# Optimization experiments

Measured on AMD Instinct MI355X. Metric: run time of the kernel, lower is better.

The kernel has to match this reference:

```python
import jax, jax.numpy as jnp
import numpy as np
import math

SPARSITY = 0.5
EPS = 1e-5


def _quant(x, bit, after_relu):
    # mirrors torch quantize_per_tensor math; straight-through (torch mutates x.data)
    def q(x):
        mx, mn = x.max(), x.min()
        scale = (mx - mn) / (2 ** bit - 1)
        if after_relu:
            ir = jnp.clip(jnp.round(x / scale), 0.0, 2 ** bit - 1)
            return ir * scale
        zp_min = jnp.floor(mn / scale)
        return (jnp.round((x - mn) / scale) + zp_min) * scale
    return x + jax.lax.stop_gradient(q(x) - x)


def _subnet(scores, k):
    # GetSubnet: top-k mask of |scores| with straight-through gradient
    s = jnp.abs(scores)
    flat = s.ravel()
    j = int((1.0 - k) * flat.size)
    order = jnp.argsort(flat)
    mask = jnp.zeros_like(flat).at[order[j:]].set(1.0).reshape(s.shape)
    return jax.lax.stop_gradient(mask - s) + s


def _scale(hw_one, fan_in):
    std = math.sqrt(2.0) / math.sqrt(fan_in * 0.5)
    return hw_one.mean() / std


def _blend_w(scores, sign, hw_one, hw_zero):
    m = _subnet(scores, SPARSITY)
    return sign * (hw_one[0] * m + hw_zero[0] * (1.0 - m))


def _conv(x, w):
    return jax.lax.conv_general_dilated(x, w, (1, 1), 'VALID',
                                        dimension_numbers=('NCHW', 'OIHW', 'NCHW'))


def _maxpool2(x):
    return jax.lax.reduce_window(x, -jnp.inf, jax.lax.max,
                                 (1, 1, 2, 2), (1, 1, 2, 2), 'VALID')


def _bn(x):
    m = x.mean((0, 2, 3), keepdims=True)
    v = x.var((0, 2, 3), keepdims=True)
    return (x - m) / jnp.sqrt(v + EPS)


def setup_inputs() -> dict:
    key = jax.random.key(0)
    ks = jax.random.split(key, 16)
    B = 4096
    shapes = {
        '1': (64, 1, 3, 3),
        '2': (16, 64, 3, 3),
        '3': (128, 400),
        '4': (10, 128),
    }
    inp = {'x': jax.random.normal(ks[0], (B, 1, 28, 28), dtype=jnp.float32)}
    i = 1
    for name, shp in shapes.items():
        inp['scores' + name] = jax.random.normal(ks[i], shp, dtype=jnp.float32); i += 1
        inp['sign' + name] = jnp.sign(jax.random.normal(ks[i], shp, dtype=jnp.float32)); i += 1
        inp['hw' + name + '_one'] = jax.random.uniform(ks[i], (1,) + shp, dtype=jnp.float32); i += 1
        # hw_zero: small "off" conductances
        inp['hw' + name + '_zero'] = 0.05 * jax.random.uniform(jax.random.fold_in(ks[i], 1), (1,) + shp, dtype=jnp.float32)
    inp['qb'] = 8
    return inp


def reference(x, scores1, sign1, hw1_one, hw1_zero,
              scores2, sign2, hw2_one, hw2_zero,
              scores3, sign3, hw3_one, hw3_zero,
              scores4, sign4, hw4_one, hw4_zero, qb):
    x = _maxpool2(x)
    x = _quant(x, qb, False)
    # conv1 (fan_in = 1*3*3 = 9)
    w1 = _blend_w(scores1, sign1, hw1_one, hw1_zero)
    x = _conv(x, w1) / _scale(hw1_one, 9)
    x = jax.nn.relu(_bn(x))
    x = _quant(x, qb, True)
    # conv2 (fan_in = 64*9 = 576)
    w2 = _blend_w(scores2, sign2, hw2_one, hw2_zero)
    x = _conv(x, w2) / _scale(hw2_one, 576)
    x = _maxpool2(x)
    x = jax.nn.relu(_bn(x))
    x = _quant(x, qb, True)
    x = x.reshape(x.shape[0], -1)  # [B, 400]
    # fc1 (fan_in = 400)
    w3 = _blend_w(scores3, sign3, hw3_one, hw3_zero)
    x = (x @ w3.T) / _scale(hw3_one, 400)
    x = jax.nn.relu(x)
    x = _quant(x, qb, True)
    # fc2 (fan_in = 128)
    w4 = _blend_w(scores4, sign4, hw4_one, hw4_zero)
    x = (x @ w4.T) / _scale(hw4_one, 128)
    return jax.nn.log_softmax(x, axis=1)
```

## Files before the change

### kernel.cpp

```cpp
#include <hip/hip_runtime.h>
#include <hip/hip_bf16.h>
#include <math.h>

#define DEV __device__ __forceinline__

constexpr int BATCH = 4096;
constexpr int NBA = 512;
constexpr int NBB = 4096;
constexpr int NBC = 4096;
constexpr int NBE = 512;
constexpr int NBW = 16;

constexpr size_t OFF_POOLED = 0;
constexpr size_t OFF_Y2P = OFF_POOLED + (size_t)BATCH*196;
constexpr size_t OFF_ST1 = OFF_Y2P;
constexpr size_t OFF_H3  = OFF_Y2P + (size_t)BATCH*400;
constexpr size_t OFF_ST2 = OFF_H3;
constexpr size_t OFF_W2  = OFF_H3 + (size_t)BATCH*128;
constexpr size_t OFF_W3  = OFF_W2 + 9216;
constexpr size_t OFF_W4  = OFF_W3 + 51200;
constexpr size_t OFF_WSC = OFF_W4 + 1280;
constexpr size_t OFF_BN1 = OFF_WSC + 4;
constexpr size_t OFF_BN2 = OFF_BN1 + 256;
constexpr size_t OFF_GMM = OFF_BN2 + 64;
constexpr size_t OFF_ONS = OFF_GMM + 8;
constexpr size_t OFF_T   = OFF_ONS + 16;
constexpr size_t OFF_MMA = OFF_T + 4;
constexpr size_t OFF_HIST= OFF_MMA + 1024;
constexpr size_t OFF_W1M = OFF_HIST + 32768;
constexpr size_t OFF_SEL = OFF_W1M + 2048;
constexpr size_t OFF_H2G = OFF_SEL + 8;
constexpr size_t OFF_H3G = OFF_H2G + 4096;

typedef __attribute__((ext_vector_type(8))) short bf16x8;
typedef __attribute__((ext_vector_type(4))) float f32x4;

struct InPtrs {
  const float* x;
  const float* sc[4];
  const float* sg[4];
  const float* on[4];
  const float* ze[4];
  const int* qb;
};

__constant__ const int KW_L[16]  ={0,1,1,2,2,2,2,2,2,2,2,2,2,2,2,3};
__constant__ const int KW_S[16]  ={0,0,1,0,1,2,3,4,5,6,7,8,9,10,11,0};
__constant__ const int KW_NB[4]  ={1,2,12,1};
__constant__ const int KW_N[4]   ={576,9216,51200,1280};
__constant__ const int KW_FAN[4] ={9,576,400,128};
__constant__ const int KW_BW0[4] ={0,1,3,15};
__constant__ const int KW_BW1[4] ={1,3,15,16};

DEV unsigned fenc(float f){ unsigned u=__float_as_uint(f); return (u&0x80000000u)? ~u : (u|0x80000000u); }
DEV float fdec(unsigned e){ return __uint_as_float((e&0x80000000u)? (e&0x7fffffffu) : ~e); }
DEV unsigned short f2bf(float f){ unsigned u=__float_as_uint(f); return (unsigned short)((u + 0x7fffu + ((u>>16)&1u))>>16); }

DEV float blk_sum(float v, float* red, int t){
  red[t]=v; __syncthreads();
  for (int s=128;s>0;s>>=1){ if(t<s) red[t]+=red[t+s]; __syncthreads(); }
  float r=red[0]; __syncthreads();
  return r;
}
DEV float blk_min(float v, float* red, int t){
  red[t]=v; __syncthreads();
  for (int s=128;s>0;s>>=1){ if(t<s) red[t]=fminf(red[t],red[t+s]); __syncthreads(); }
  float r=red[0]; __syncthreads();
  return r;
}
DEV float blk_max(float v, float* red, int t){
  red[t]=v; __syncthreads();
  for (int s=128;s>0;s>>=1){ if(t<s) red[t]=fmaxf(red[t],red[t+s]); __syncthreads(); }
  float r=red[0]; __syncthreads();
  return r;
}

DEV int2 find256(const int* hist, int nbins, int kk, int t, int* suf, int* sh2){
  const int G=nbins>>8;
  const int lo=t*G;
  int g=0;
  for (int b=0;b<G;++b) g+=hist[lo+b];
  suf[t]=g; __syncthreads();
  for (int s=1;s<256;s<<=1){
    int add=(t+s<256)?suf[t+s]:0;
    __syncthreads();
    suf[t]+=add;
    __syncthreads();
  }
  const int S=suf[t];
  const int Snext=(t<255)?suf[t+1]:0;
  if (S>=kk && Snext<kk){
    int c2=Snext;
    for (int b=lo+G-1;b>=lo;--b){
      c2+=hist[b];
      if (c2>=kk){ sh2[0]=b; sh2[1]=kk-(c2-hist[b]); break; }
    }
  }
  __syncthreads();
  int2 r=make_int2(sh2[0],sh2[1]);
  __syncthreads();
  return r;
}

DEV void build_pat(unsigned* PAT, const unsigned short* qxs, int t){
  for (int pos=t; pos<144; pos+=256){
    int py=(pos*171)>>11;
    int px=pos-py*12;
    const unsigned short* q0=qxs+py*16+px;
    unsigned e0=q0[0],  e1=q0[1],  e2=q0[2];
    unsigned e3=q0[16], e4=q0[17], e5=q0[18];
    unsigned e6=q0[32], e7=q0[33], e8=q0[34];
    uint4* dst=(uint4*)(PAT+pos*20);
    dst[0]=make_uint4(e0|(e1<<16), e2|(e3<<16), e4|(e5<<16), e6|(e7<<16));
    dst[1]=make_uint4(e8, 0u, 0u, 0u);
    dst[2]=make_uint4(0u,0u,0u,0u);
    dst[3]=make_uint4(0u,0u,0u,0u);
  }
}

__global__ __launch_bounds__(256) void ka_kernel(InPtrs in, float* __restrict__ ws){
  const int t=threadIdx.x, blk=blockIdx.x;
  __shared__ int h[2048];
  __shared__ float red[256];
  if (blk<NBA){
    if (blk==0){
      unsigned* Z=(unsigned*)(ws+OFF_H2G);
      for (int i=t;i<8192;i+=256) Z[i]=0u;
    }
    const float* x=in.x;
    float* pooled=ws+OFF_POOLED;
    float lmn=3.4e38f, lmx=-3.4e38f;
    for (int p=blk*256+t; p<BATCH*196; p+=NBA*256){
      int b=p/196, r=p-b*196;
      int oy=r/14, ox=r-oy*14;
      const float* px=x+b*784+oy*56+ox*2;
      float m=fmaxf(fmaxf(px[0],px[1]),fmaxf(px[28],px[29]));
      pooled[p]=m;
      lmn=fminf(lmn,m); lmx=fmaxf(lmx,m);
    }
    float bmn=blk_min(lmn,red,t);
    float bmx=blk_max(lmx,red,t);
    if (t==0){ ws[OFF_MMA+blk*2]=bmn; ws[OFF_MMA+blk*2+1]=bmx; }
  } else {
    const int bw=blk-NBA;
    const int L=KW_L[bw], s=KW_S[bw], nb=KW_NB[L];
    const int n4=KW_N[L]>>2;
    const int lo=(int)(((long long)n4*s)/nb), hi=(int)(((long long)n4*(s+1))/nb);
    const float4* sc4=(const float4*)in.sc[L];
    const float4* on4=(const float4*)in.on[L];
    for (int i=t;i<2048;i+=256) h[i]=0;
    __syncthreads();
    float onsum=0.f;
    for (int i=lo+t;i<hi;i+=256){
      float4 v=sc4[i];
      atomicAdd(&h[(__float_as_uint(v.x)&0x7fffffffu)>>20],1);
      atomicAdd(&h[(__float_as_uint(v.y)&0x7fffffffu)>>20],1);
      atomicAdd(&h[(__float_as_uint(v.z)&0x7fffffffu)>>20],1);
      atomicAdd(&h[(__float_as_uint(v.w)&0x7fffffffu)>>20],1);
      float4 o=on4[i];
      onsum+=(o.x+o.y)+(o.z+o.w);
    }
    __syncthreads();
    unsigned* GH=(unsigned*)(ws+OFF_HIST);
    for (int i=t;i<2048;i+=256) GH[bw*2048+i]=(unsigned)h[i];
    float S=blk_sum(onsum,red,t);
    if (t==0) ws[OFF_ONS+bw]=S;
  }
}

__global__ __launch_bounds__(256) void kw2a_kernel(float* __restrict__ ws){
  const int t=threadIdx.x, L=blockIdx.x;
  __shared__ int hist[2048];
  __shared__ int suf[256];
  __shared__ int sh2[2];
  __shared__ float redm[256], redx[256];
  if (L==0){
    float a0=ws[OFF_MMA+2*t],       a1=ws[OFF_MMA+2*(t+256)];
    float b0=ws[OFF_MMA+2*t+1],     b1=ws[OFF_MMA+2*(t+256)+1];
    redm[t]=fminf(a0,a1); redx[t]=fmaxf(b0,b1);
    __syncthreads();
    for (int s=128;s>0;s>>=1){
      if (t<s){ redm[t]=fminf(redm[t],redm[t+s]); redx[t]=fmaxf(redx[t],redx[t+s]); }
      __syncthreads();
    }
    unsigned* U=(unsigned*)(ws+OFF_GMM);
    if (t==0){ U[0]=fenc(redm[0]); U[1]=fenc(redx[0]); }
    if (t>=2 && t<8) U[t]=(t&1)? 0u : 0xFFFFFFFFu;
    unsigned* z=(unsigned*)(ws+OFF_W1M);
    for (int i=t;i<2048;i+=256) z[i]=0u;
    __syncthreads();
  }
  const unsigned* GH=(const unsigned*)(ws+OFF_HIST);
  for (int i=t;i<2048;i+=256){
    int s=0;
    for (int bw=KW_BW0[L]; bw<KW_BW1[L]; ++bw) s+=(int)GH[bw*2048+i];
    hist[i]=s;
  }
  __syncthreads();
  int2 f1=find256(hist,2048,KW_N[L]>>1,t,suf,sh2);
  if (t==0){
    unsigned* SEL=(unsigned*)(ws+OFF_SEL);
    SEL[L*2]=(unsigned)f1.x; SEL[L*2+1]=(unsigned)f1.y;
  }
}

__global__ __launch_bounds__(256) void kwp2_kernel(InPtrs in, float* __restrict__ ws){
  const int t=threadIdx.x, bw=blockIdx.x;
  const int L=KW_L[bw], s=KW_S[bw], nb=KW_NB[L];
  const int n4=KW_N[L]>>2;
  const int lo=(int)(((long long)n4*s)/nb), hi=(int)(((long long)n4*(s+1))/nb);
  const unsigned b0=((const unsigned*)(ws+OFF_SEL))[L*2];
  const float4* sc4=(const float4*)in.sc[L];
  unsigned* GH2=(unsigned*)(ws+OFF_H2G)+L*1024;
  for (int i=lo+t;i<hi;i+=256){
    float4 v=sc4[i];
    unsigned ux=__float_as_uint(v.x)&0x7fffffffu;
    unsigned uy=__float_as_uint(v.y)&0x7fffffffu;
    unsigned uz=__float_as_uint(v.z)&0x7fffffffu;
    unsigned uw=__float_as_uint(v.w)&0x7fffffffu;
    if ((ux>>20)==b0) atomicAdd(&GH2[(ux>>10)&1023u],1u);
    if ((uy>>20)==b0) atomicAdd(&GH2[(uy>>10)&1023u],1u);
    if ((uz>>20)==b0) atomicAdd(&GH2[(uz>>10)&1023u],1u);
    if ((uw>>20)==b0) atomicAdd(&GH2[(uw>>10)&1023u],1u);
  }
}

__global__ __launch_bounds__(256) void kwp3_kernel(InPtrs in, float* __restrict__ ws){
  const int t=threadIdx.x, bw=blockIdx.x;
  const int L=KW_L[bw], s=KW_S[bw], nb=KW_NB[L];
  const int n4=KW_N[L]>>2;
  const int lo=(int)(((long long)n4*s)/nb), hi=(int)(((long long)n4*(s+1))/nb);
  const unsigned* SEL=(const unsigned*)(ws+OFF_SEL);
  const unsigned b0=SEL[L*2]; const int r1=(int)SEL[L*2+1];
  __shared__ int hist[1024];
  __shared__ int suf[256];
  __shared__ int sh2[2];
  const unsigned* GH2=(const unsigned*)(ws+OFF_H2G)+L*1024;
  for (int i=t;i<1024;i+=256) hist[i]=(int)GH2[i];
  __syncthreads();
  int2 f2=find256(hist,1024,r1,t,suf,sh2);
  const unsigned pre=(b0<<10)|(unsigned)f2.x;
  const float4* sc4=(const float4*)in.sc[L];
  unsigned* GH3=(unsigned*)(ws+OFF_H3G)+L*1024;
  for (int i=lo+t;i<hi;i+=256){
    float4 v=sc4[i];
    unsigned ux=__float_as_uint(v.x)&0x7fffffffu;
    unsigned uy=__float_as_uint(v.y)&0x7fffffffu;
    unsigned uz=__float_as_uint(v.z)&0x7fffffffu;
    unsigned uw=__float_as_uint(v.w)&0x7fffffffu;
    if ((ux>>10)==pre) atomicAdd(&GH3[ux&1023u],1u);
    if ((uy>>10)==pre) atomicAdd(&GH3[uy&1023u],1u);
    if ((uz>>10)==pre) atomicAdd(&GH3[uz&1023u],1u);
    if ((uw>>10)==pre) atomicAdd(&GH3[uw&1023u],1u);
  }
}

__global__ __launch_bounds__(256) void kw3_kernel(InPtrs in, float* __restrict__ ws){
  const int t=threadIdx.x, bw=blockIdx.x;
  const int L=KW_L[bw], s=KW_S[bw], nb=KW_NB[L];
  const int n4=KW_N[L]>>2;
  const int lo=(int)(((long long)n4*s)/nb), hi=(int)(((long long)n4*(s+1))/nb);
  const unsigned* SEL=(const unsigned*)(ws+OFF_SEL);
  const unsigned b0=SEL[L*2]; const int r1=(int)SEL[L*2+1];
  __shared__ int hist[1024];
  __shared__ int suf[256];
  __shared__ int sh2[2];
  const unsigned* GH2=(const unsigned*)(ws+OFF_H2G)+L*1024;
  for (int i=t;i<1024;i+=256) hist[i]=(int)GH2[i];
  __syncthreads();
  int2 f2=find256(hist,1024,r1,t,suf,sh2);
  const unsigned pre=(b0<<10)|(unsigned)f2.x;
  const int r2=f2.y;
  __syncthreads();
  const unsigned* GH3=(const unsigned*)(ws+OFF_H3G)+L*1024;
  for (int i=t;i<1024;i+=256) hist[i]=(int)GH3[i];
  __syncthreads();
  int2 f3=find256(hist,1024,r2,t,suf,sh2);
  const unsigned T=(pre<<10)|(unsigned)f3.x;
  if (s==0 && t==0){
    float os=0.f;
    for (int b=KW_BW0[L]; b<KW_BW1[L]; ++b) os+=ws[OFF_ONS+b];
    ws[OFF_WSC+L]=(os/(float)KW_N[L])*sqrtf((float)KW_FAN[L])*0.5f;
  }
  const float4* sc4=(const float4*)in.sc[L];
  const float4* sg4=(const float4*)in.sg[L];
  const float4* on4=(const float4*)in.on[L];
  const float4* ze4=(const float4*)in.ze[L];
  float* wout=ws+OFF_W4;
  unsigned* W3Fu=(unsigned*)(ws+OFF_W3);
  unsigned short* W1F=(unsigned short*)(ws+OFF_W1M);
  unsigned short* W2F=(unsigned short*)(ws+OFF_W2);
  for (int i4=lo+t;i4<hi;i4+=256){
    float4 sv4=sc4[i4], g=sg4[i4], o=on4[i4], z=ze4[i4];
    float sv[4]={sv4.x,sv4.y,sv4.z,sv4.w}, gv[4]={g.x,g.y,g.z,g.w};
    float ov[4]={o.x,o.y,o.z,o.w}, zv[4]={z.x,z.y,z.z,z.w};
    #pragma unroll
    for (int j=0;j<4;++j){
      int i=i4*4+j;
      unsigned u=__float_as_uint(sv[j])&0x7fffffffu;
      float w=gv[j]*((u>=T)? ov[j] : zv[j]);
      if (L==0){
        int oc=i/9; int k=i-oc*9;
        int ocT=oc>>4, ocL=oc&15, quad=k>>3, kj=k&7;
        unsigned short hb=f2bf(w);
        float lo2=w-__uint_as_float((unsigned)hb<<16);
        W1F[((((ocT*2+0)*4+quad)*16+ocL)<<3)+kj]=hb;
        W1F[((((ocT*2+1)*4+quad)*16+ocL)<<3)+kj]=f2bf(lo2);
      } else if (L==1){
        int oc=i/576; int r=i-oc*576; int ic=r/9; int kp=r-ic*9;
        int ss=ic>>5, rem=ic&31, quad=rem>>3, kj=rem&7;
        unsigned short hb=f2bf(w);
        float lo2=w-__uint_as_float((unsigned)hb<<16);
        W2F[(((((kp*2+ss)*2+0)*4+quad)*16+oc)<<3)+kj]=hb;
        W2F[(((((kp*2+ss)*2+1)*4+quad)*16+oc)<<3)+kj]=f2bf(lo2);
      } else if (L==2){
        int oc=i/400; int kk=i-oc*400;
        unsigned short hb=f2bf(w);
        float lo2=w-__uint_as_float((unsigned)hb<<16);
        unsigned short lb=f2bf(lo2);
        int ct=oc>>4, l15=oc&15;
        unsigned idx=((unsigned)((kk>>4)*8+ct)*64u + (unsigned)(((kk>>2)&3)*16+l15))*4u + (unsigned)(kk&3);
        W3Fu[idx]=(unsigned)hb | ((unsigned)lb<<16);
      } else {
        wout[i]=w;
      }
    }
  }
}

__global__ __launch_bounds__(256) void kb_kernel(InPtrs in, const float* __restrict__ wsr, float* __restrict__ wsw){
  const int t=threadIdx.x, blk=blockIdx.x;
  __shared__ unsigned short qxs[256];
  __shared__ __align__(16) unsigned PAT[2880];
  __shared__ float xw[1024];
  const float* pooled=wsr+OFF_POOLED;
  const unsigned* U=(const unsigned*)(wsr+OFF_GMM);
  const float mn0=fdec(U[0]);
  const float mx0=fdec(U[1]);
  const float lvf=(float)((1<<in.qb[0])-1);
  const float s0=(mx0-mn0)/lvf, inv_s0=1.0f/s0, zp0=floorf(mn0/s0);
  const float sv=s0/wsr[OFF_WSC+0];
  if (t<224){
    int row=t>>4, col=t&15;
    float q=0.f;
    if (col<14){ float xx=pooled[(size_t)blk*196+row*14+col]; q=rintf((xx-mn0)*inv_s0)+zp0; }
    qxs[t]=(unsigned short)(__float_as_uint(q)>>16);
  }
  __syncthreads();
  build_pat(PAT,qxs,t);
  __syncthreads();
  {
    const int w=t>>6, lane=t&63;
    const int l15=lane&15, quad=lane>>4;
    const unsigned short* W1F=(const unsigned short*)(wsr+OFF_W1M);
    const unsigned short* PATu=(const unsigned short*)PAT;
    #pragma unroll
    for (int ocT=0; ocT<4; ++ocT){
      bf16x8 bh=*(const bf16x8*)(W1F+(((ocT*2+0)*64+lane)<<3));
      bf16x8 bl=*(const bf16x8*)(W1F+(((ocT*2+1)*64+lane)<<3));
      float sum=0.f,sq=0.f,mn=3.4e38f,mx=-3.4e38f;
      for (int tl=w; tl<9; tl+=4){
        bf16x8 a=*(const bf16x8*)(PATu+(tl*16+l15)*40+quad*8);
        f32x4 acc=(f32x4){0.f,0.f,0.f,0.f};
        acc=__builtin_amdgcn_mfma_f32_16x16x32_bf16(a,bh,acc,0,0,0);
        acc=__builtin_amdgcn_mfma_f32_16x16x32_bf16(a,bl,acc,0,0,0);
        #pragma unroll
        for (int r=0;r<4;++r){
          float v=acc[r]*sv;
          sum+=v; sq=fmaf(v,v,sq); mn=fminf(mn,v); mx=fmaxf(mx,v);
        }
      }
      #pragma unroll
      for (int d=16;d<64;d<<=1){
        sum+=__shfl_xor(sum,d);
        sq +=__shfl_xor(sq,d);
        mn=fminf(mn,__shfl_xor(mn,d));
        mx=fmaxf(mx,__shfl_xor(mx,d));
      }
      if (quad==0){
        float* p=xw+((w*4+ocT)*16+l15)*4;
        p[0]=sum; p[1]=sq; p[2]=mn; p[3]=mx;
      }
    }
  }
  __syncthreads();
  if (t<64){
    float sum=0.f,sq=0.f,mn=3.4e38f,mx=-3.4e38f;
    #pragma unroll
    for (int w=0;w<4;++w){
      const float* p=xw+((w*4+(t>>4))*16+(t&15))*4;
      sum+=p[0]; sq+=p[1]; mn=fminf(mn,p[2]); mx=fmaxf(mx,p[3]);
    }
    float* p=wsw+OFF_ST1+((size_t)t*NBB+blk)*4;
    p[0]=sum; p[1]=sq; p[2]=mn; p[3]=mx;
  }
}

__global__ __launch_bounds__(256) void kstat_kernel(const float* __restrict__ wsr, float* __restrict__ wsw,
                                                    unsigned long long inoff, int nparts, float Nf,
                                                    unsigned long long outoff, int mmslot){
  const int c=blockIdx.x, t=threadIdx.x;
  __shared__ float red[256];
  const float* p=wsr+inoff+(size_t)c*nparts*4;
  float sum=0.f,sq=0.f,mn=3.4e38f,mx=-3.4e38f;
  for (int i=t;i<nparts;i+=256){
    sum+=p[i*4]; sq+=p[i*4+1];
    mn=fminf(mn,p[i*4+2]); mx=fmaxf(mx,p[i*4+3]);
  }
  float S=blk_sum(sum,red,t);
  float Q=blk_sum(sq,red,t);
  float MN=blk_min(mn,red,t);
  float MX=blk_max(mx,red,t);
  if (t==0){
    float mean=S/Nf;
    float var=fmaxf(Q/Nf-mean*mean,0.f);
    float sd=sqrtf(var+1e-5f);
    float* o=wsw+outoff+c*4;
    float tmn=(MN-mean)/sd, tmx=(MX-mean)/sd;
    o[0]=mean; o[1]=sd; o[2]=tmn; o[3]=tmx;
    unsigned* U=(unsigned*)(wsw+OFF_GMM);
    atomicMin(&U[mmslot],fenc(tmn));
    atomicMax(&U[mmslot+1],fenc(tmx));
  }
}

__global__ __launch_bounds__(256) void kc_kernel(InPtrs in, const float* __restrict__ wsr, float* __restrict__ wsw){
  const int t=threadIdx.x, blk=blockIdx.x;
  __shared__ unsigned short qxs[256];
  __shared__ __align__(16) unsigned PAT[2880];
  __shared__ __align__(16) unsigned short actA[144*72];
  __shared__ float sA2[64], sB2[64];
  float* c2s=(float*)PAT;
  const float* pooled=wsr+OFF_POOLED;
  const unsigned* U=(const unsigned*)(wsr+OFF_GMM);
  const float mn0=fdec(U[0]);
  const float mx0=fdec(U[1]);
  const float rmn=fdec(U[2]);
  const float rmx=fdec(U[3]);
  const float lvf=(float)((1<<in.qb[0])-1);
  const float s0=(mx0-mn0)/lvf, inv_s0=1.0f/s0, zp0=floorf(mn0/s0);
  const float s1w=wsr[OFF_WSC+0], s2w=wsr[OFF_WSC+1];
  const float s2=(fmaxf(rmx,0.f)-fmaxf(rmn,0.f))/lvf;
  const float inv_s2=1.0f/s2;
  const float g2=s2/s2w;
  if (t<64){
    float m=wsr[OFF_BN1+t*4], sd=wsr[OFF_BN1+t*4+1];
    sA2[t]=s0/(s1w*sd);
    sB2[t]=-m/sd;
  }
  if (t<224){
    int row=t>>4, col=t&15;
    float q=0.f;
    if (col<14){ float xx=pooled[(size_t)blk*196+row*14+col]; q=rintf((xx-mn0)*inv_s0)+zp0; }
    qxs[t]=(unsigned short)(__float_as_uint(q)>>16);
  }
  __syncthreads();
  build_pat(PAT,qxs,t);
  __syncthreads();
  {
    const int w=t>>6, lane=t&63;
    const int l15=lane&15, quad=lane>>4;
    const unsigned short* W1F=(const unsigned short*)(wsr+OFF_W1M);
    const unsigned short* PATu=(const unsigned short*)PAT;
    #pragma unroll
    for (int ocT=0; ocT<4; ++ocT){
      bf16x8 bh=*(const bf16x8*)(W1F+(((ocT*2+0)*64+lane)<<3));
      bf16x8 bl=*(const bf16x8*)(W1F+(((ocT*2+1)*64+lane)<<3));
      const int oc=ocT*16+l15;
      const float a2=sA2[oc], b2=sB2[oc];
      for (int tl=w; tl<9; tl+=4){
        bf16x8 a=*(const bf16x8*)(PATu+(tl*16+l15)*40+quad*8);
        f32x4 acc=(f32x4){0.f,0.f,0.f,0.f};
        acc=__builtin_amdgcn_mfma_f32_16x16x32_bf16(a,bh,acc,0,0,0);
        acc=__builtin_amdgcn_mfma_f32_16x16x32_bf16(a,bl,acc,0,0,0);
        #pragma unroll
        for (int r=0;r<4;++r){
          int pos=tl*16+quad*4+r;
          float f=fminf(rintf(fmaxf(fmaf(acc[r],a2,b2),0.f)*inv_s2),lvf);
          actA[pos*72+oc]=(unsigned short)(__float_as_uint(f)>>16);
        }
      }
    }
  }
  __syncthreads();
  {
    const int w=t>>6, lane=t&63;
    const int oc=lane&15, quad=lane>>4;
    const unsigned short* W2F=(const unsigned short*)(wsr+OFF_W2);
    const int nT=(w<3)?2:1;
    int abase[2]; int taus[2];
    for (int i=0;i<nT;++i){
      int tau=w+i*4;
      int posb=tau*16+(lane&15);
      int pc=posb>99?99:posb;
      int py=pc/10, px=pc-py*10;
      abase[i]=(py*12+px)*72+quad*8;
      taus[i]=tau;
    }
    f32x4 acc[2];
    acc[0]=(f32x4){0.f,0.f,0.f,0.f};
    acc[1]=(f32x4){0.f,0.f,0.f,0.f};
    #pragma unroll 3
    for (int kykx=0;kykx<9;++kykx){
      const int co=((kykx/3)*12+(kykx%3))*72;
      #pragma unroll
      for (int s=0;s<2;++s){
        bf16x8 bh=*(const bf16x8*)(W2F+((((kykx*2+s)*2+0)*64+lane)<<3));
        bf16x8 bl=*(const bf16x8*)(W2F+((((kykx*2+s)*2+1)*64+lane)<<3));
        #pragma unroll
        for (int i=0;i<2;++i){
          if (i<nT){
            bf16x8 a=*(const bf16x8*)(actA+abase[i]+co+s*32);
            acc[i]=__builtin_amdgcn_mfma_f32_16x16x32_bf16(a,bh,acc[i],0,0,0);
            acc[i]=__builtin_amdgcn_mfma_f32_16x16x32_bf16(a,bl,acc[i],0,0,0);
          }
        }
      }
    }
    __syncthreads();
    for (int i=0;i<nT;++i){
      int pos4=taus[i]*16+quad*4;
      if (pos4<100){
        float4* dst=(float4*)&c2s[oc*100+pos4];
        *dst=make_float4(acc[i].x*g2,acc[i].y*g2,acc[i].z*g2,acc[i].w*g2);
      }
    }
  }
  __syncthreads();
  for (int i=t;i<400;i+=256){
    int ch=i/25, pp=i-ch*25;
    int py=pp/5, px=pp-py*5;
    const float* cc=c2s+ch*100;
    int base=py*20+px*2;
    float v=fmaxf(fmaxf(cc[base],cc[base+1]),fmaxf(cc[base+10],cc[base+11]));
    wsw[OFF_Y2P+(size_t)blk*400+i]=v;
  }
  {
    const int ch=t>>4, g=t&15;
    float sum=0.f,sq=0.f,mn=3.4e38f,mx=-3.4e38f;
    const float* cc=c2s+ch*100;
    for (int j=g;j<25;j+=16){
      int py=j/5, px=j-py*5;
      int base=py*20+px*2;
      float v=fmaxf(fmaxf(cc[base],cc[base+1]),fmaxf(cc[base+10],cc[base+11]));
      sum+=v; sq=fmaf(v,v,sq); mn=fminf(mn,v); mx=fmaxf(mx,v);
    }
    #pragma unroll
    for (int d=1;d<16;d<<=1){
      sum+=__shfl_xor(sum,d);
      sq +=__shfl_xor(sq,d);
      mn=fminf(mn,__shfl_xor(mn,d));
      mx=fmaxf(mx,__shfl_xor(mx,d));
    }
    if (g==0){
      float* p=wsw+OFF_ST2+((size_t)ch*NBC+blk)*4;
      p[0]=sum; p[1]=sq; p[2]=mn; p[3]=mx;
    }
  }
}

__global__ __launch_bounds__(256) void ke_kernel(InPtrs in, const float* __restrict__ wsr, float* __restrict__ wsw){
  const int t=threadIdx.x, blk=blockIdx.x;
  __shared__ __align__(16) unsigned short xs[16*808];
  __shared__ float sm[16], sisd[16];
  __shared__ float rwn[4], rwx[4];
  const unsigned* U=(const unsigned*)(wsr+OFF_GMM);
  const float lvf=(float)((1<<in.qb[0])-1);
  const float rmn=fdec(U[4]);
  const float rmx=fdec(U[5]);
  if (t<16){ sm[t]=wsr[OFF_BN2+t*4]; sisd[t]=1.0f/wsr[OFF_BN2+t*4+1]; }
  const float s3=(fmaxf(rmx,0.f)-fmaxf(rmn,0.f))/lvf;
  const float inv_s3=1.0f/s3;
  const float inv_s3w=1.0f/wsr[OFF_WSC+2];
  const int b0=(blk>>1)*16;
  __syncthreads();
  {
    const int img=t>>4, tg=t&15;
    const float* yrow=wsr+OFF_Y2P+(size_t)(b0+img)*400;
    unsigned* xsu=(unsigned*)xs;
    for (int n=0;n<25;++n){
      int k=n*16+tg;
      int ch=k/25;
      float y=yrow[k];
      float r=fmaxf((y-sm[ch])*sisd[ch],0.f);
      float q=fminf(rintf(r*inv_s3),lvf);
      unsigned qb=__float_as_uint(q)>>16;
      xsu[img*404+k]=qb|(qb<<16);
    }
  }
  __syncthreads();
  const int w=t>>6, lane=t&63, l15=lane&15, quad=lane>>4;
  const int ct=(blk&1)*4+w;
  const bf16x8* Wf=(const bf16x8*)(wsr+OFF_W3);
  const unsigned short* arow=xs+l15*808;
  f32x4 acc=(f32x4){0.f,0.f,0.f,0.f};
  #pragma unroll 5
  for (int kt=0;kt<25;++kt){
    bf16x8 a=*(const bf16x8*)(arow+kt*32+quad*8);
    bf16x8 b=Wf[(kt*8+ct)*64+lane];
    acc=__builtin_amdgcn_mfma_f32_16x16x32_bf16(a,b,acc,0,0,0);
  }
  const float scale=s3*inv_s3w;
  float hmn=3.4e38f,hmx=-3.4e38f;
  #pragma unroll
  for (int r=0;r<4;++r){
    float h=fmaxf(acc[r]*scale,0.f);
    wsw[OFF_H3+(size_t)(b0+quad*4+r)*128+ct*16+l15]=h;
    hmn=fminf(hmn,h); hmx=fmaxf(hmx,h);
  }
  #pragma unroll
  for (int d=1;d<64;d<<=1){
    hmn=fminf(hmn,__shfl_xor(hmn,d));
    hmx=fmaxf(hmx,__shfl_xor(hmx,d));
  }
  if (lane==0){ rwn[w]=hmn; rwx[w]=hmx; }
  __syncthreads();
  if (t==0){
    float mn=fminf(fminf(rwn[0],rwn[1]),fminf(rwn[2],rwn[3]));
    float mx=fmaxf(fmaxf(rwx[0],rwx[1]),fmaxf(rwx[2],rwx[3]));
    float* p=wsw+OFF_MMA+(size_t)blk*2;
    p[0]=mn; p[1]=mx;
  }
}

__global__ __launch_bounds__(256) void kf_kernel(InPtrs in, const float* __restrict__ wsr, float* __restrict__ out){
  const int t=threadIdx.x, blk=blockIdx.x;
  __shared__ float w4s[1280];
  __shared__ float redn[256], redxs[256];
  const float lvf=(float)((1<<in.qb[0])-1);
  for (int i=t;i<1280;i+=256) w4s[i]=wsr[OFF_W4+i];
  {
    const float* mmp=wsr+OFF_MMA;
    float mn=3.4e38f, mx=-3.4e38f;
    for (int i=t;i<NBE;i+=256){
      mn=fminf(mn,mmp[2*i]);
      mx=fmaxf(mx,mmp[2*i+1]);
    }
    redn[t]=mn; redxs[t]=mx;
    __syncthreads();
    for (int s=128;s>0;s>>=1){
      if (t<s){ redn[t]=fminf(redn[t],redn[t+s]); redxs[t]=fmaxf(redxs[t],redxs[t+s]); }
      __syncthreads();
    }
  }
  const float hmn=redn[0];
  const float hmx=redxs[0];
  const float s4=(hmx-hmn)/lvf;
  const float inv_s4=1.0f/s4;
  const float inv_s4w=1.0f/wsr[OFF_WSC+3];
  const int row=blk*64+(t>>2), l4=t&3;
  const float4* hr4=(const float4*)(wsr+OFF_H3+(size_t)row*128);
  float acc[10];
  #pragma unroll
  for (int j=0;j<10;++j) acc[j]=0.f;
  #pragma unroll 2
  for (int j=0;j<8;++j){
    float4 v=hr4[l4*8+j];
    int kb=(l4*8+j)*4;
    float q0=fminf(rintf(v.x*inv_s4),lvf)*s4;
    float q1=fminf(rintf(v.y*inv_s4),lvf)*s4;
    float q2=fminf(rintf(v.z*inv_s4),lvf)*s4;
    float q3=fminf(rintf(v.w*inv_s4),lvf)*s4;
    #pragma unroll
    for (int o=0;o<10;++o){
      const float* wr=w4s+o*128+kb;
      acc[o]=fmaf(q0,wr[0],acc[o]);
      acc[o]=fmaf(q1,wr[1],acc[o]);
      acc[o]=fmaf(q2,wr[2],acc[o]);
      acc[o]=fmaf(q3,wr[3],acc[o]);
    }
  }
  #pragma unroll
  for (int o=0;o<10;++o){
    acc[o]+=__shfl_xor(acc[o],1);
    acc[o]+=__shfl_xor(acc[o],2);
  }
  if (l4==0){
    float mx=-3.4e38f;
    #pragma unroll
    for (int o=0;o<10;++o){ acc[o]*=inv_s4w; mx=fmaxf(mx,acc[o]); }
    float se=0.f;
    #pragma unroll
    for (int o=0;o<10;++o) se+=expf(acc[o]-mx);
    const float ls=logf(se);
    #pragma unroll
    for (int o=0;o<10;++o) out[row*10+o]=acc[o]-mx-ls;
  }
}

extern "C" void kernel_launch(void* const* d_in, const int* in_sizes, int n_in,
                              void* d_out, int out_size, void* d_ws, size_t ws_size,
                              hipStream_t stream){
  (void)in_sizes; (void)n_in; (void)out_size; (void)ws_size;
  InPtrs P;
  P.x=(const float*)d_in[0];
  for (int l=0;l<4;++l){
    P.sc[l]=(const float*)d_in[1+l*4];
    P.sg[l]=(const float*)d_in[2+l*4];
    P.on[l]=(const float*)d_in[3+l*4];
    P.ze[l]=(const float*)d_in[4+l*4];
  }
  P.qb=(const int*)d_in[17];
  float* ws=(float*)d_ws;

  hipLaunchKernelGGL(ka_kernel,   dim3(NBA+NBW), dim3(256), 0, stream, P, ws);
  hipLaunchKernelGGL(kw2a_kernel, dim3(4),       dim3(256), 0, stream, ws);
  hipLaunchKernelGGL(kwp2_kernel, dim3(NBW),     dim3(256), 0, stream, P, ws);
  hipLaunchKernelGGL(kwp3_kernel, dim3(NBW),     dim3(256), 0, stream, P, ws);
  hipLaunchKernelGGL(kw3_kernel,  dim3(NBW),     dim3(256), 0, stream, P, ws);
  hipLaunchKernelGGL(kb_kernel,   dim3(NBB),     dim3(256), 0, stream, P, ws, ws);
  hipLaunchKernelGGL(kstat_kernel, dim3(64), dim3(256), 0, stream, ws, ws,
                     (unsigned long long)OFF_ST1, NBB, 4096.f*144.f, (unsigned long long)OFF_BN1, 2);
  hipLaunchKernelGGL(kc_kernel,   dim3(NBC),     dim3(256), 0, stream, P, ws, ws);
  hipLaunchKernelGGL(kstat_kernel, dim3(16), dim3(256), 0, stream, ws, ws,
                     (unsigned long long)OFF_ST2, NBC, 4096.f*25.f, (unsigned long long)OFF_BN2, 4);
  hipLaunchKernelGGL(ke_kernel,   dim3(NBE),     dim3(256), 0, stream, P, ws, ws);
  hipLaunchKernelGGL(kf_kernel,   dim3(64),      dim3(256), 0, stream, P, ws, (float*)d_out);
}
```

Measured before the change: 239.3 us.

## Split conv2 MFMA work by K across wave pairs and pad activation LDS layout

Conv1 MFMA operands are swapped so that each lane holds four consecutive output channels and writes them as one packed 8-byte LDS store instead of four scalar stores. Conv2 work is repartitioned: waves are paired, each pair covering four position tiles, and the nine kernel taps are split between the two waves of a pair. The two partial sums are written to separate LDS buffers and added during the pooling pass. The activation row stride grows from 72 to 88 halves, which is meant to reduce LDS bank conflicts. The cost is a larger LDS footprint and an extra add per pooled element.

```diff
diff --git a/kernel.cpp b/kernel.cpp
--- a/kernel.cpp
+++ b/kernel.cpp
@@ -427,10 +427,11 @@
 __global__ __launch_bounds__(256) void kc_kernel(InPtrs in, const float* __restrict__ wsr, float* __restrict__ wsw){
   const int t=threadIdx.x, blk=blockIdx.x;
   __shared__ unsigned short qxs[256];
-  __shared__ __align__(16) unsigned PAT[2880];
-  __shared__ __align__(16) unsigned short actA[144*72];
+  __shared__ __align__(16) unsigned PATBUF[3328];
+  __shared__ __align__(16) unsigned short actA[144*88];
   __shared__ float sA2[64], sB2[64];
-  float* c2s=(float*)PAT;
+  unsigned* PAT=PATBUF;
+  float (*c2sP)[16][104]=(float(*)[16][104])PATBUF;
   const float* pooled=wsr+OFF_POOLED;
   const unsigned* U=(const unsigned*)(wsr+OFF_GMM);
   const float mn0=fdec(U[0]);
@@ -457,93 +458,113 @@
   __syncthreads();
   build_pat(PAT,qxs,t);
   __syncthreads();
+  const int w=t>>6, lane=t&63;
+  const int l15=lane&15, quad=lane>>4;
   {
-    const int w=t>>6, lane=t&63;
-    const int l15=lane&15, quad=lane>>4;
     const unsigned short* W1F=(const unsigned short*)(wsr+OFF_W1M);
     const unsigned short* PATu=(const unsigned short*)PAT;
     #pragma unroll
     for (int ocT=0; ocT<4; ++ocT){
       bf16x8 bh=*(const bf16x8*)(W1F+(((ocT*2+0)*64+lane)<<3));
       bf16x8 bl=*(const bf16x8*)(W1F+(((ocT*2+1)*64+lane)<<3));
-      const int oc=ocT*16+l15;
-      const float a2=sA2[oc], b2=sB2[oc];
+      const int oc0=ocT*16+quad*4;
+      const float a20=sA2[oc0],   b20=sB2[oc0];
+      const float a21=sA2[oc0+1], b21=sB2[oc0+1];
+      const float a22=sA2[oc0+2], b22=sB2[oc0+2];
+      const float a23=sA2[oc0+3], b23=sB2[oc0+3];
       for (int tl=w; tl<9; tl+=4){
         bf16x8 a=*(const bf16x8*)(PATu+(tl*16+l15)*40+quad*8);
         f32x4 acc=(f32x4){0.f,0.f,0.f,0.f};
-        acc=__builtin_amdgcn_mfma_f32_16x16x32_bf16(a,bh,acc,0,0,0);
-        acc=__builtin_amdgcn_mfma_f32_16x16x32_bf16(a,bl,acc,0,0,0);
-        #pragma unroll
-        for (int r=0;r<4;++r){
-          int pos=tl*16+quad*4+r;
-          float f=fminf(rintf(fmaxf(fmaf(acc[r],a2,b2),0.f)*inv_s2),lvf);
-          actA[pos*72+oc]=(unsigned short)(__float_as_uint(f)>>16);
-        }
+        acc=__builtin_amdgcn_mfma_f32_16x16x32_bf16(bh,a,acc,0,0,0);
+        acc=__builtin_amdgcn_mfma_f32_16x16x32_bf16(bl,a,acc,0,0,0);
+        const int pos=tl*16+l15;
+        float f0=fminf(rintf(fmaxf(fmaf(acc[0],a20,b20),0.f)*inv_s2),lvf);
+        float f1=fminf(rintf(fmaxf(fmaf(acc[1],a21,b21),0.f)*inv_s2),lvf);
+        float f2v=fminf(rintf(fmaxf(fmaf(acc[2],a22,b22),0.f)*inv_s2),lvf);
+        float f3=fminf(rintf(fmaxf(fmaf(acc[3],a23,b23),0.f)*inv_s2),lvf);
+        unsigned w0=(__float_as_uint(f0)>>16)|((__float_as_uint(f1)>>16)<<16);
+        unsigned w1=(__float_as_uint(f2v)>>16)|((__float_as_uint(f3)>>16)<<16);
+        *(uint2*)(actA+pos*88+oc0)=make_uint2(w0,w1);
       }
     }
   }
   __syncthreads();
   {
-    const int w=t>>6, lane=t&63;
-    const int oc=lane&15, quad=lane>>4;
+    const int wm=w>>1, wk=w&1;
+    const int k0=wk?5:0, nK=wk?4:5;
+    const int nT2=wm?3:4;
     const unsigned short* W2F=(const unsigned short*)(wsr+OFF_W2);
-    const int nT=(w<3)?2:1;
-    int abase[2]; int taus[2];
-    for (int i=0;i<nT;++i){
-      int tau=w+i*4;
-      int posb=tau*16+(lane&15);
+    int abase[4];
+    #pragma unroll
+    for (int i=0;i<4;++i){
+      int tau=wm*4+i;
+      int posb=tau*16+l15;
       int pc=posb>99?99:posb;
       int py=pc/10, px=pc-py*10;
-      abase[i]=(py*12+px)*72+quad*8;
-      taus[i]=tau;
-    }
-    f32x4 acc[2];
+      abase[i]=(py*12+px)*176+quad*16;
+    }
+    f32x4 acc[4];
     acc[0]=(f32x4){0.f,0.f,0.f,0.f};
     acc[1]=(f32x4){0.f,0.f,0.f,0.f};
-    #pragma unroll 3
-    for (int kykx=0;kykx<9;++kykx){
-      const int co=((kykx/3)*12+(kykx%3))*72;
-      #pragma unroll
-      for (int s=0;s<2;++s){
-        bf16x8 bh=*(const bf16x8*)(W2F+((((kykx*2+s)*2+0)*64+lane)<<3));
-        bf16x8 bl=*(const bf16x8*)(W2F+((((kykx*2+s)*2+1)*64+lane)<<3));
+    acc[2]=(f32x4){0.f,0.f,0.f,0.f};
+    acc[3]=(f32x4){0.f,0.f,0.f,0.f};
+    const char* actB=(const char*)actA;
+    #pragma unroll
+    for (int kk=0;kk<5;++kk){
+      if (kk<nK){
+        int kykx=k0+kk;
+        int ky=(kykx*11)>>5;
+        int kx=kykx-ky*3;
+        int co=(ky*12+kx)*176;
         #pragma unroll
-        for (int i=0;i<2;++i){
-          if (i<nT){
-            bf16x8 a=*(const bf16x8*)(actA+abase[i]+co+s*32);
-            acc[i]=__builtin_amdgcn_mfma_f32_16x16x32_bf16(a,bh,acc[i],0,0,0);
-            acc[i]=__builtin_amdgcn_mfma_f32_16x16x32_bf16(a,bl,acc[i],0,0,0);
+        for (int s=0;s<2;++s){
+          bf16x8 bh=*(const bf16x8*)(W2F+((((kykx*2+s)*2+0)*64+lane)<<3));
+          bf16x8 bl=*(const bf16x8*)(W2F+((((kykx*2+s)*2+1)*64+lane)<<3));
+          #pragma unroll
+          for (int i=0;i<4;++i){
+            if (i<nT2){
+              bf16x8 a=*(const bf16x8*)(actB+abase[i]+co+s*64);
+              acc[i]=__builtin_amdgcn_mfma_f32_16x16x32_bf16(a,bh,acc[i],0,0,0);
+              acc[i]=__builtin_amdgcn_mfma_f32_16x16x32_bf16(a,bl,acc[i],0,0,0);
+            }
           }
         }
       }
     }
-    __syncthreads();
-    for (int i=0;i<nT;++i){
-      int pos4=taus[i]*16+quad*4;
-      if (pos4<100){
-        float4* dst=(float4*)&c2s[oc*100+pos4];
-        *dst=make_float4(acc[i].x*g2,acc[i].y*g2,acc[i].z*g2,acc[i].w*g2);
+    #pragma unroll
+    for (int i=0;i<4;++i){
+      if (i<nT2){
+        int pos4=(wm*4+i)*16+quad*4;
+        if (pos4<100){
+          float4* dst=(float4*)&c2sP[wk][l15][pos4];
+          *dst=make_float4(acc[i].x*g2,acc[i].y*g2,acc[i].z*g2,acc[i].w*g2);
+        }
       }
     }
   }
   __syncthreads();
-  for (int i=t;i<400;i+=256){
-    int ch=i/25, pp=i-ch*25;
-    int py=pp/5, px=pp-py*5;
-    const float* cc=c2s+ch*100;
-    int base=py*20+px*2;
-    float v=fmaxf(fmaxf(cc[base],cc[base+1]),fmaxf(cc[base+10],cc[base+11]));
-    wsw[OFF_Y2P+(size_t)blk*400+i]=v;
-  }
   {
     const int ch=t>>4, g=t&15;
+    const float* cc0=&c2sP[0][ch][0];
+    const float* cc1=&c2sP[1][ch][0];
     float sum=0.f,sq=0.f,mn=3.4e38f,mx=-3.4e38f;
-    const float* cc=c2s+ch*100;
-    for (int j=g;j<25;j+=16){
-      int py=j/5, px=j-py*5;
-      int base=py*20+px*2;
-      float v=fmaxf(fmaxf(cc[base],cc[base+1]),fmaxf(cc[base+10],cc[base+11]));
-      sum+=v; sq=fmaf(v,v,sq); mn=fminf(mn,v); mx=fmaxf(mx,v);
+    #pragma unroll
+    for (int it=0;it<2;++it){
+      int j=g+it*16;
+      if (j<25){
+        int py=(j*52)>>8;
+        int px=j-py*5;
+        int base=py*20+px*2;
+        float2 p0=*(const float2*)(cc0+base);
+        float2 p1=*(const float2*)(cc0+base+10);
+        float2 q0=*(const float2*)(cc1+base);
+        float2 q1=*(const float2*)(cc1+base+10);
+        float a0=p0.x+q0.x, a1=p0.y+q0.y;
+        float b0=p1.x+q1.x, b1=p1.y+q1.y;
+        float v=fmaxf(fmaxf(a0,a1),fmaxf(b0,b1));
+        wsw[OFF_Y2P+(size_t)blk*400+ch*25+j]=v;
+        sum+=v; sq=fmaf(v,v,sq); mn=fminf(mn,v); mx=fmaxf(mx,v);
+      }
     }
     #pragma unroll
     for (int d=1;d<16;d<<=1){
```

Result: faster. 232.8 us (-2.7%).
